# Performance work log

Hardware: AMD Instinct MI355X
Metric: run time of the kernel (lower is better)

## Reference

```python
import jax, jax.numpy as jnp
import numpy as np

N_IN = 512
N_OUT = 256
K = 3
GRID_SIZE = N_OUT - K + 1  # 254
X_LO, X_HI = -1.0, 1.0
BATCH = 1024
LN_EPS = 1e-5


def make_grid():
    # grid_values: (n_in, grid_size + 2k + 1), identical rows as in the torch module
    step = (X_HI - X_LO) / GRID_SIZE
    g = jnp.linspace(X_LO - step * K, X_HI + step * K, GRID_SIZE + 2 * K + 1, dtype=jnp.float32)
    return jnp.broadcast_to(g, (N_IN, g.shape[0]))


def setup_inputs() -> dict:
    key = jax.random.key(0)
    k1, k2, k3 = jax.random.split(key, 3)
    x = jax.random.normal(k1, (BATCH, N_IN), dtype=jnp.float32)
    # kaiming-uniform-like scale for the linear weights
    weights = jax.random.normal(k2, (N_OUT, N_IN), dtype=jnp.float32) * (1.0 / np.sqrt(N_IN))
    spline_weights = jax.random.normal(k3, (N_OUT, N_IN, GRID_SIZE + K), dtype=jnp.float32) * (
        1.0 / np.sqrt(N_IN * (GRID_SIZE + K))
    )
    prelu_a = jnp.full((1,), 0.25, dtype=jnp.float32)  # PReLU default init
    return {"x": x, "weights": weights, "spline_weights": spline_weights, "prelu_a": prelu_a}


def reference(x, weights, spline_weights, prelu_a):
    g = make_grid()  # (n_in, P) with P = GRID_SIZE + 2K + 1
    # base branch: tanh(x) @ W^T
    b_out = jnp.tanh(x) @ weights.T  # (B, n_out)

    # Cox-de Boor recursion for B-spline bases
    xe = x[:, :, None]  # (B, n_in, 1)
    bases = ((xe >= g[:, :-1]) & (xe < g[:, 1:])).astype(x.dtype)  # (B, n_in, P-1)
    for k in range(1, K + 1):
        left = g[:, : -(k + 1)]
        right = g[:, k:-1]
        delta = jnp.where(right == left, jnp.ones_like(right), right - left)
        bases = (xe - left) / delta * bases[:, :, :-1] + (
            (g[:, k + 1 :] - xe) / (g[:, k + 1 :] - g[:, 1:-k])
        ) * bases[:, :, 1:]
    # bases: (B, n_in, GRID_SIZE + K)

    # flattened linear == einsum over (n_in, grid) axes
    spline_out = jnp.einsum("big,oig->bo", bases, spline_weights)  # (B, n_out)

    y = b_out + spline_out
    # LayerNorm without affine params
    mu = jnp.mean(y, axis=-1, keepdims=True)
    var = jnp.var(y, axis=-1, keepdims=True)
    yn = (y - mu) / jnp.sqrt(var + LN_EPS)
    # PReLU (single shared slope)
    return jnp.where(yn >= 0, yn, prelu_a[0] * yn)
```

## Files before the change

kernel.cpp:

```cpp
#include <hip/hip_runtime.h>
#include <hip/hip_fp16.h>
#include <math.h>

#define N_IN   512
#define N_OUT  256
#define NCOEF  257
#define BATCH  1024
#define LN_EPS 1e-5f
#define G0F (-1.0f - 3.0f * (2.0f / 254.0f))

#define ROWQ 20
#define NQ   129
#define SLABW (NQ * ROWQ)

#define SLOT(q_, oo_) ((q_) * ROWQ + (((((oo_) >> 2) ^ ((q_) & 3))) << 2) + ((oo_) & 3))

static __device__ __forceinline__ unsigned pk_bf16x2(float a, float b) {
    unsigned ua = ((__float_as_uint(a) + 0x8000u) >> 16) & 0xffffu;
    unsigned ub = (__float_as_uint(b) + 0x8000u) & 0xffff0000u;
    return ua | ub;
}

static __device__ __forceinline__ float dot2bf(unsigned w, unsigned s, float c) {
    float d;
    asm("v_dot2_f32_bf16 %0, %1, %2, %3" : "=v"(d) : "v"(w), "v"(s), "v"(c));
    return d;
}

static __device__ __forceinline__ uint4 spline_pack(float xv) {
    const float e2 = __expf(2.f * xv);
    const float tx = 1.f - 2.f / (e2 + 1.f);
    const float u  = (xv - G0F) * 127.f;
    const bool has = (u >= 0.f) && (u < 260.f);
    const float uf = has ? u : 0.f;
    int m = (int)uf;
    if (m > 259) m = 259;
    const float tt = uf - (float)m;
    const float t2 = tt * tt, t3 = t2 * tt;
    const float omt = 1.f - tt;
    float a0 = omt * omt * omt * (1.f / 6.f);
    float a1 = (3.f * t3 - 6.f * t2 + 4.f) * (1.f / 6.f);
    float a2 = (-3.f * t3 + 3.f * t2 + 3.f * tt + 1.f) * (1.f / 6.f);
    float a3 = t3 * (1.f / 6.f);
    if (!has) { a0 = a1 = a2 = a3 = 0.f; }
    const int pb  = m - 3;
    const int pbc = pb < 0 ? 0 : (pb > 253 ? 253 : pb);
    const int d   = pbc - pb;
    if (d >= 1)  { a0 = a1; a1 = a2; a2 = a3; a3 = 0.f; }
    if (d >= 2)  { a0 = a1; a1 = a2; a2 = a3; a3 = 0.f; }
    if (d >= 3)  { a0 = a1; a1 = a2; a2 = a3; a3 = 0.f; }
    if (d <= -1) { a3 = a2; a2 = a1; a1 = a0; a0 = 0.f; }
    if (d <= -2) { a3 = a2; a2 = a1; a1 = a0; a0 = 0.f; }
    if (d <= -3) { a3 = a2; a2 = a1; a1 = a0; a0 = 0.f; }
    uint4 r;
    if (pbc & 1) {
        r.x = pk_bf16x2(0.f, a0);
        r.y = pk_bf16x2(a1, a2);
        r.z = pk_bf16x2(a3, 0.f);
    } else {
        r.x = pk_bf16x2(a0, a1);
        r.y = pk_bf16x2(a2, a3);
        r.z = 0u;
    }
    r.w = (unsigned)(pbc & ~1) |
          ((unsigned)__half_as_ushort(__float2half(tx)) << 16);
    return r;
}

__global__ __launch_bounds__(512, 4) void kan_main(
    const float* __restrict__ x, const float* __restrict__ W,
    const float* __restrict__ sw, float* __restrict__ part)
{
    const int bid = blockIdx.x;
    const int bc = bid & 1;
    const int oc = (bid >> 1) & 15;
    const int ig = bid >> 5;
    const int o0 = oc * 16, i0 = ig * 32, b0 = bc * 512;
    const int t = threadIdx.x;

    __shared__ __align__(16) unsigned slab[2][2][SLABW];

    const int soo = t & 15;
    const int sgc = t >> 4;

    const float* swrow = sw + ((size_t)(o0 + soo) * N_IN + i0) * NCOEF;
    const float* xp    = x + (size_t)(b0 + t) * N_IN + i0;

    float4 A0, B0, A1, B1;
    float t0 = 0.f, t1 = 0.f;
    float2 xc, xn, x2;

#define GLOAD(p) do {                                             \
        const float* _r0 = swrow + (size_t)(2 * (p)) * NCOEF;     \
        const float* _r1 = _r0 + NCOEF;                           \
        A0 = *(const float4*)&_r0[sgc * 4];                       \
        B0 = *(const float4*)&_r0[sgc * 4 + 128];                 \
        A1 = *(const float4*)&_r1[sgc * 4];                       \
        B1 = *(const float4*)&_r1[sgc * 4 + 128];                 \
        if (sgc == 31) { t0 = _r0[256]; t1 = _r1[256]; }          \
    } while (0)

#define STAGE(wb) do {                                            \
        unsigned* _s0 = &slab[wb][0][0];                          \
        unsigned* _s1 = &slab[wb][1][0];                          \
        const int _qa = 2 * sgc;                                  \
        _s0[SLOT(_qa,      soo)] = pk_bf16x2(A0.x, A0.y);         \
        _s0[SLOT(_qa + 1,  soo)] = pk_bf16x2(A0.z, A0.w);         \
        _s0[SLOT(_qa + 64, soo)] = pk_bf16x2(B0.x, B0.y);         \
        _s0[SLOT(_qa + 65, soo)] = pk_bf16x2(B0.z, B0.w);         \
        _s1[SLOT(_qa,      soo)] = pk_bf16x2(A1.x, A1.y);         \
        _s1[SLOT(_qa + 1,  soo)] = pk_bf16x2(A1.z, A1.w);         \
        _s1[SLOT(_qa + 64, soo)] = pk_bf16x2(B1.x, B1.y);         \
        _s1[SLOT(_qa + 65, soo)] = pk_bf16x2(B1.z, B1.w);         \
        if (sgc == 31) {                                          \
            _s0[SLOT(128, soo)] = pk_bf16x2(t0, 0.f);             \
            _s1[SLOT(128, soo)] = pk_bf16x2(t1, 0.f);             \
        }                                                         \
    } while (0)

    float acc[16];
#pragma unroll
    for (int oo = 0; oo < 16; ++oo) acc[oo] = 0.f;

    GLOAD(0);
    xc = *(const float2*)&xp[0];
    STAGE(0);
    GLOAD(1);
    xn = *(const float2*)&xp[2];
    x2 = xn;
    __syncthreads();

    int buf = 0;
    for (int n = 0; n < 16; ++n) {
        if (n + 1 < 16) {
            STAGE(buf ^ 1);
            if (n + 2 < 16) {
                GLOAD(n + 2);
                x2 = *(const float2*)&xp[2 * (n + 2)];
            }
        }

#pragma unroll
        for (int sub = 0; sub < 2; ++sub) {
            const int i = i0 + 2 * n + sub;
            const uint4 u = spline_pack(sub == 0 ? xc.x : xc.y);
            const float tx =
                __half2float(__ushort_as_half((unsigned short)(u.w >> 16)));
            const float* Wrow = W + (size_t)o0 * N_IN + i;
#pragma unroll
            for (int oo = 0; oo < 16; ++oo)
                acc[oo] = fmaf(tx, Wrow[(size_t)oo * N_IN], acc[oo]);
            if (u.x | u.y | u.z) {
                const int q0 = (int)(u.w & 0xffffu) >> 1;
                const unsigned* sl = &slab[buf][sub][0];
#pragma unroll
                for (int j = 0; j < 3; ++j) {
                    const int q = q0 + j;
                    const unsigned wj = (j == 0) ? u.x : (j == 1) ? u.y : u.z;
                    const unsigned* row = sl + q * ROWQ;
                    const int m = q & 3;
#pragma unroll
                    for (int lq = 0; lq < 4; ++lq) {
                        const uint4 s4 = *(const uint4*)&row[(lq ^ m) << 2];
                        acc[lq * 4 + 0] = dot2bf(wj, s4.x, acc[lq * 4 + 0]);
                        acc[lq * 4 + 1] = dot2bf(wj, s4.y, acc[lq * 4 + 1]);
                        acc[lq * 4 + 2] = dot2bf(wj, s4.z, acc[lq * 4 + 2]);
                        acc[lq * 4 + 3] = dot2bf(wj, s4.w, acc[lq * 4 + 3]);
                    }
                }
            }
        }

        __syncthreads();
        buf ^= 1;
        xc = xn;
        xn = x2;
    }

    float* dst = part + ((size_t)ig * BATCH + b0 + t) * N_OUT + o0;
#pragma unroll
    for (int v = 0; v < 4; ++v)
        *reinterpret_cast<float4*>(&dst[v * 4]) =
            make_float4(acc[v * 4], acc[v * 4 + 1], acc[v * 4 + 2], acc[v * 4 + 3]);
#undef GLOAD
#undef STAGE
}

__global__ __launch_bounds__(256) void kan_ln(
    const float* __restrict__ part, const float* __restrict__ prelu_a,
    float* __restrict__ out)
{
    const int b = blockIdx.x;
    const int t = threadIdx.x;

    float sv = 0.f;
#pragma unroll
    for (int k = 0; k < 16; ++k)
        sv += part[((size_t)k * BATCH + b) * N_OUT + t];

    float v1 = sv, v2 = sv * sv;
#pragma unroll
    for (int d = 1; d < 64; d <<= 1) {
        v1 += __shfl_xor(v1, d);
        v2 += __shfl_xor(v2, d);
    }
    __shared__ float r1[4], r2[4];
    if ((t & 63) == 0) { r1[t >> 6] = v1; r2[t >> 6] = v2; }
    __syncthreads();
    const float tot1 = r1[0] + r1[1] + r1[2] + r1[3];
    const float tot2 = r2[0] + r2[1] + r2[2] + r2[3];

    const float mu  = tot1 * (1.f / N_OUT);
    const float var = tot2 * (1.f / N_OUT) - mu * mu;
    const float inv = rsqrtf(var + LN_EPS);
    const float yn  = (sv - mu) * inv;
    const float a   = prelu_a[0];
    out[(size_t)b * N_OUT + t] = (yn >= 0.f) ? yn : a * yn;
}

extern "C" void kernel_launch(void* const* d_in, const int* in_sizes, int n_in,
                              void* d_out, int out_size, void* d_ws, size_t ws_size,
                              hipStream_t stream)
{
    const float* x  = (const float*)d_in[0];
    const float* W  = (const float*)d_in[1];
    const float* sw = (const float*)d_in[2];
    const float* pa = (const float*)d_in[3];
    float* out  = (float*)d_out;
    float* part = (float*)d_ws;

    kan_main<<<dim3(512), 512, 0, stream>>>(x, W, sw, part);
    kan_ln  <<<dim3(1024), 256, 0, stream>>>(part, pa, out);
}
```

Baseline: 98.46 us.

## Split output columns across lane quads and broadcast spline bases via DPP

Each thread used to own one batch row and all 16 outputs. Now each group of 4 lanes shares 4 batch rows, and each lane owns 4 output columns. The spline basis values of each lane in a quad are broadcast to the others with DPP quad-permutes, so each thread reads one 16-byte LDS vector per coefficient row instead of four. Linear-branch weights are staged in shared memory alongside the spline slab rather than read per thread from global memory. This lowers LDS traffic and register accumulators per thread, at the cost of extra DPP moves, four serial branches per input, and more divergence within a wavefront.

```diff
diff --git a/kernel.cpp b/kernel.cpp
--- a/kernel.cpp
+++ b/kernel.cpp
@@ -14,6 +14,8 @@
 #define SLABW (NQ * ROWQ)
 
 #define SLOT(q_, oo_) ((q_) * ROWQ + (((((oo_) >> 2) ^ ((q_) & 3))) << 2) + ((oo_) & 3))
+
+#define QP(v_, C_) ((unsigned)__builtin_amdgcn_mov_dpp((int)(v_), (C_), 0xf, 0xf, true))
 
 static __device__ __forceinline__ unsigned pk_bf16x2(float a, float b) {
     unsigned ua = ((__float_as_uint(a) + 0x8000u) >> 16) & 0xffffu;
@@ -79,15 +81,18 @@
     const int t = threadIdx.x;
 
     __shared__ __align__(16) unsigned slab[2][2][SLABW];
-
+    __shared__ float Wl[2][2][16];
+
+    const int wv = t >> 6, bl = (t >> 2) & 15, og = t & 3;
     const int soo = t & 15;
     const int sgc = t >> 4;
 
     const float* swrow = sw + ((size_t)(o0 + soo) * N_IN + i0) * NCOEF;
-    const float* xp    = x + (size_t)(b0 + t) * N_IN + i0;
+    const float* xp  = x + (size_t)(b0 + wv * 64 + og * 16 + bl) * N_IN + i0;
+    const float* wgp = W + (size_t)(o0 + (t & 15)) * N_IN + i0 + (t >> 4);
 
     float4 A0, B0, A1, B1;
-    float t0 = 0.f, t1 = 0.f;
+    float t0 = 0.f, t1 = 0.f, Wc = 0.f;
     float2 xc, xn, x2;
 
 #define GLOAD(p) do {                                             \
@@ -118,15 +123,46 @@
         }                                                         \
     } while (0)
 
-    float acc[16];
-#pragma unroll
-    for (int oo = 0; oo < 16; ++oo) acc[oo] = 0.f;
+#define DO_BP(bp_, CTRL_) do {                                                \
+        uint4 ub;                                                             \
+        ub.x = QP(u.x, CTRL_); ub.y = QP(u.y, CTRL_);                         \
+        ub.z = QP(u.z, CTRL_); ub.w = QP(u.w, CTRL_);                         \
+        const float tx =                                                      \
+            __half2float(__ushort_as_half((unsigned short)(ub.w >> 16)));     \
+        float4 a = acc[bp_];                                                  \
+        a.x = fmaf(tx, Wv.x, a.x);                                            \
+        a.y = fmaf(tx, Wv.y, a.y);                                            \
+        a.z = fmaf(tx, Wv.z, a.z);                                            \
+        a.w = fmaf(tx, Wv.w, a.w);                                            \
+        if (ub.x | ub.y | ub.z) {                                             \
+            const int q0 = (int)(ub.w & 0xffffu) >> 1;                        \
+            _Pragma("unroll")                                                 \
+            for (int j = 0; j < 3; ++j) {                                     \
+                const int q = q0 + j;                                         \
+                const unsigned wj = (j == 0) ? ub.x : (j == 1) ? ub.y : ub.z; \
+                const uint4 s4 =                                              \
+                    *(const uint4*)&sl[q * ROWQ + ((og ^ (q & 3)) << 2)];     \
+                a.x = dot2bf(wj, s4.x, a.x);                                  \
+                a.y = dot2bf(wj, s4.y, a.y);                                  \
+                a.z = dot2bf(wj, s4.z, a.z);                                  \
+                a.w = dot2bf(wj, s4.w, a.w);                                  \
+            }                                                                 \
+        }                                                                     \
+        acc[bp_] = a;                                                         \
+    } while (0)
+
+    float4 acc[4];
+#pragma unroll
+    for (int bp = 0; bp < 4; ++bp) acc[bp] = make_float4(0.f, 0.f, 0.f, 0.f);
 
     GLOAD(0);
     xc = *(const float2*)&xp[0];
+    if (t < 32) Wc = wgp[0];
     STAGE(0);
+    if (t < 32) Wl[0][t >> 4][t & 15] = Wc;
     GLOAD(1);
     xn = *(const float2*)&xp[2];
+    if (t < 32) Wc = wgp[2];
     x2 = xn;
     __syncthreads();
 
@@ -134,41 +170,23 @@
     for (int n = 0; n < 16; ++n) {
         if (n + 1 < 16) {
             STAGE(buf ^ 1);
+            if (t < 32) Wl[buf ^ 1][t >> 4][t & 15] = Wc;
             if (n + 2 < 16) {
                 GLOAD(n + 2);
                 x2 = *(const float2*)&xp[2 * (n + 2)];
+                if (t < 32) Wc = wgp[2 * (n + 2)];
             }
         }
 
 #pragma unroll
         for (int sub = 0; sub < 2; ++sub) {
-            const int i = i0 + 2 * n + sub;
             const uint4 u = spline_pack(sub == 0 ? xc.x : xc.y);
-            const float tx =
-                __half2float(__ushort_as_half((unsigned short)(u.w >> 16)));
-            const float* Wrow = W + (size_t)o0 * N_IN + i;
-#pragma unroll
-            for (int oo = 0; oo < 16; ++oo)
-                acc[oo] = fmaf(tx, Wrow[(size_t)oo * N_IN], acc[oo]);
-            if (u.x | u.y | u.z) {
-                const int q0 = (int)(u.w & 0xffffu) >> 1;
-                const unsigned* sl = &slab[buf][sub][0];
-#pragma unroll
-                for (int j = 0; j < 3; ++j) {
-                    const int q = q0 + j;
-                    const unsigned wj = (j == 0) ? u.x : (j == 1) ? u.y : u.z;
-                    const unsigned* row = sl + q * ROWQ;
-                    const int m = q & 3;
-#pragma unroll
-                    for (int lq = 0; lq < 4; ++lq) {
-                        const uint4 s4 = *(const uint4*)&row[(lq ^ m) << 2];
-                        acc[lq * 4 + 0] = dot2bf(wj, s4.x, acc[lq * 4 + 0]);
-                        acc[lq * 4 + 1] = dot2bf(wj, s4.y, acc[lq * 4 + 1]);
-                        acc[lq * 4 + 2] = dot2bf(wj, s4.z, acc[lq * 4 + 2]);
-                        acc[lq * 4 + 3] = dot2bf(wj, s4.w, acc[lq * 4 + 3]);
-                    }
-                }
-            }
+            const float4 Wv = *(const float4*)&Wl[buf][sub][og << 2];
+            const unsigned* sl = &slab[buf][sub][0];
+            DO_BP(0, 0x00);
+            DO_BP(1, 0x55);
+            DO_BP(2, 0xAA);
+            DO_BP(3, 0xFF);
         }
 
         __syncthreads();
@@ -177,13 +195,14 @@
         xn = x2;
     }
 
-    float* dst = part + ((size_t)ig * BATCH + b0 + t) * N_OUT + o0;
-#pragma unroll
-    for (int v = 0; v < 4; ++v)
-        *reinterpret_cast<float4*>(&dst[v * 4]) =
-            make_float4(acc[v * 4], acc[v * 4 + 1], acc[v * 4 + 2], acc[v * 4 + 3]);
+    float* dst = part + ((size_t)ig * BATCH + b0 + wv * 64 + bl) * N_OUT
+               + o0 + (og << 2);
+#pragma unroll
+    for (int bp = 0; bp < 4; ++bp)
+        *reinterpret_cast<float4*>(&dst[(size_t)bp * 16 * N_OUT]) = acc[bp];
 #undef GLOAD
 #undef STAGE
+#undef DO_BP
 }
 
 __global__ __launch_bounds__(256) void kan_ln(
```

Result: slower. 106.6 us (+8.3%).

## Remap threads to batch×output-group tiles, sharing packed spline weights via LDS

Applied to the files above, without the earlier changes.

Each thread now covers 4 batch rows × 4 outputs instead of 1 batch row × 16 outputs. Per-input spline packs are computed once per batch row and shared through LDS, and W columns are staged in LDS instead of being reloaded from global per thread. This removes the 16 strided W global loads per input and cuts LDS reads, since each thread now reads one uint4 per basis instead of four. The cost is extra LDS traffic for the packed bases and more divergence, because the four batch rows in a thread take different branches on the zero-basis check.

```diff
diff --git a/kernel.cpp b/kernel.cpp
--- a/kernel.cpp
+++ b/kernel.cpp
@@ -79,16 +79,20 @@
     const int t = threadIdx.x;
 
     __shared__ __align__(16) unsigned slab[2][2][SLABW];
-
+    __shared__ __align__(16) uint4 wpk[2][512];
+    __shared__ float Wl[2][2][16];
+
+    const int wv = t >> 6;
+    const int bl = (t >> 2) & 15, og = t & 3;
     const int soo = t & 15;
     const int sgc = t >> 4;
 
     const float* swrow = sw + ((size_t)(o0 + soo) * N_IN + i0) * NCOEF;
     const float* xp    = x + (size_t)(b0 + t) * N_IN + i0;
+    const float* wgp   = W + (size_t)(o0 + (t & 15)) * N_IN + i0 + (t >> 4);
 
     float4 A0, B0, A1, B1;
-    float t0 = 0.f, t1 = 0.f;
-    float2 xc, xn, x2;
+    float t0 = 0.f, t1 = 0.f, Wc = 0.f;
 
 #define GLOAD(p) do {                                             \
         const float* _r0 = swrow + (size_t)(2 * (p)) * NCOEF;     \
@@ -118,70 +122,92 @@
         }                                                         \
     } while (0)
 
-    float acc[16];
-#pragma unroll
-    for (int oo = 0; oo < 16; ++oo) acc[oo] = 0.f;
+    float4 acc[4];
+#pragma unroll
+    for (int bp = 0; bp < 4; ++bp) acc[bp] = make_float4(0.f, 0.f, 0.f, 0.f);
 
     GLOAD(0);
-    xc = *(const float2*)&xp[0];
+    float2 xc = *(const float2*)&xp[0];
+    if (t < 32) Wc = wgp[0];
     STAGE(0);
+    if (t < 32) Wl[0][t >> 4][t & 15] = Wc;
+    wpk[0][t] = spline_pack(xc.x);
+    wpk[1][t] = spline_pack(xc.y);
     GLOAD(1);
-    xn = *(const float2*)&xp[2];
-    x2 = xn;
+    float2 xn = *(const float2*)&xp[2];
+    if (t < 32) Wc = wgp[2];
     __syncthreads();
 
-    int buf = 0;
     for (int n = 0; n < 16; ++n) {
+        const int buf = n & 1;
+
+#pragma unroll
+        for (int sub = 0; sub < 2; ++sub) {
+            const float4 Wv = *(const float4*)&Wl[buf][sub][og << 2];
+            const unsigned* sl = &slab[buf][sub][0];
+#pragma unroll
+            for (int bp = 0; bp < 4; ++bp) {
+                const uint4 u = wpk[sub][wv * 64 + (bp << 4) + bl];
+                const float tx =
+                    __half2float(__ushort_as_half((unsigned short)(u.w >> 16)));
+                float4 a = acc[bp];
+                a.x = fmaf(tx, Wv.x, a.x);
+                a.y = fmaf(tx, Wv.y, a.y);
+                a.z = fmaf(tx, Wv.z, a.z);
+                a.w = fmaf(tx, Wv.w, a.w);
+                if (u.x | u.y | u.z) {
+                    const int q0 = (int)(u.w & 0xffffu) >> 1;
+                    {
+                        const uint4 s4 =
+                            *(const uint4*)&sl[q0 * ROWQ + ((og ^ (q0 & 3)) << 2)];
+                        a.x = dot2bf(u.x, s4.x, a.x);
+                        a.y = dot2bf(u.x, s4.y, a.y);
+                        a.z = dot2bf(u.x, s4.z, a.z);
+                        a.w = dot2bf(u.x, s4.w, a.w);
+                    }
+                    {
+                        const int q = q0 + 1;
+                        const uint4 s4 =
+                            *(const uint4*)&sl[q * ROWQ + ((og ^ (q & 3)) << 2)];
+                        a.x = dot2bf(u.y, s4.x, a.x);
+                        a.y = dot2bf(u.y, s4.y, a.y);
+                        a.z = dot2bf(u.y, s4.z, a.z);
+                        a.w = dot2bf(u.y, s4.w, a.w);
+                    }
+                    if (u.z) {
+                        const int q = q0 + 2;
+                        const uint4 s4 =
+                            *(const uint4*)&sl[q * ROWQ + ((og ^ (q & 3)) << 2)];
+                        a.x = dot2bf(u.z, s4.x, a.x);
+                        a.y = dot2bf(u.z, s4.y, a.y);
+                        a.z = dot2bf(u.z, s4.z, a.z);
+                        a.w = dot2bf(u.z, s4.w, a.w);
+                    }
+                }
+                acc[bp] = a;
+            }
+        }
+
         if (n + 1 < 16) {
             STAGE(buf ^ 1);
+            if (t < 32) Wl[buf ^ 1][t >> 4][t & 15] = Wc;
+            wpk[0][t] = spline_pack(xn.x);
+            wpk[1][t] = spline_pack(xn.y);
             if (n + 2 < 16) {
                 GLOAD(n + 2);
-                x2 = *(const float2*)&xp[2 * (n + 2)];
+                xn = *(const float2*)&xp[2 * (n + 2)];
+                if (t < 32) Wc = wgp[2 * (n + 2)];
             }
         }
-
-#pragma unroll
-        for (int sub = 0; sub < 2; ++sub) {
-            const int i = i0 + 2 * n + sub;
-            const uint4 u = spline_pack(sub == 0 ? xc.x : xc.y);
-            const float tx =
-                __half2float(__ushort_as_half((unsigned short)(u.w >> 16)));
-            const float* Wrow = W + (size_t)o0 * N_IN + i;
-#pragma unroll
-            for (int oo = 0; oo < 16; ++oo)
-                acc[oo] = fmaf(tx, Wrow[(size_t)oo * N_IN], acc[oo]);
-            if (u.x | u.y | u.z) {
-                const int q0 = (int)(u.w & 0xffffu) >> 1;
-                const unsigned* sl = &slab[buf][sub][0];
-#pragma unroll
-                for (int j = 0; j < 3; ++j) {
-                    const int q = q0 + j;
-                    const unsigned wj = (j == 0) ? u.x : (j == 1) ? u.y : u.z;
-                    const unsigned* row = sl + q * ROWQ;
-                    const int m = q & 3;
-#pragma unroll
-                    for (int lq = 0; lq < 4; ++lq) {
-                        const uint4 s4 = *(const uint4*)&row[(lq ^ m) << 2];
-                        acc[lq * 4 + 0] = dot2bf(wj, s4.x, acc[lq * 4 + 0]);
-                        acc[lq * 4 + 1] = dot2bf(wj, s4.y, acc[lq * 4 + 1]);
-                        acc[lq * 4 + 2] = dot2bf(wj, s4.z, acc[lq * 4 + 2]);
-                        acc[lq * 4 + 3] = dot2bf(wj, s4.w, acc[lq * 4 + 3]);
-                    }
-                }
-            }
-        }
-
         __syncthreads();
-        buf ^= 1;
-        xc = xn;
-        xn = x2;
-    }
-
-    float* dst = part + ((size_t)ig * BATCH + b0 + t) * N_OUT + o0;
-#pragma unroll
-    for (int v = 0; v < 4; ++v)
-        *reinterpret_cast<float4*>(&dst[v * 4]) =
-            make_float4(acc[v * 4], acc[v * 4 + 1], acc[v * 4 + 2], acc[v * 4 + 3]);
+    }
+
+    float* dst = part + ((size_t)ig * BATCH + b0) * N_OUT + o0 + (og << 2);
+#pragma unroll
+    for (int bp = 0; bp < 4; ++bp) {
+        const int lb = wv * 64 + (bp << 4) + bl;
+        *reinterpret_cast<float4*>(&dst[(size_t)lb * N_OUT]) = acc[bp];
+    }
 #undef GLOAD
 #undef STAGE
 }
```

Result: slower. 102.0 us (+3.6%).
